# Performance work log

Hardware: AMD Instinct MI355X
Metric: run time of the kernel (lower is better)

The kernel has to match this reference:

```python
import jax, jax.numpy as jnp
import numpy as np

QK = 64
KNN = 16
EPS = 1e-5


def conv1(x, w, b):
    # x: (B,C,N), w: (O,C) -> (B,O,N)
    return jnp.einsum('oc,bcn->bon', w, x) + b[None, :, None]


def conv2(x, w, b):
    # x: (B,C,N,k), w: (O,C) -> (B,O,N,k)
    return jnp.einsum('oc,bcnk->bonk', w, x) + b[None, :, None, None]


def bn1(x, g, b, m, v):
    return g[None, :, None] * (x - m[None, :, None]) * jax.lax.rsqrt(v + EPS)[None, :, None] + b[None, :, None]


def bn2(x, g, b, m, v):
    return g[None, :, None, None] * (x - m[None, :, None, None]) * jax.lax.rsqrt(v + EPS)[None, :, None, None] + b[None, :, None, None]


def gather_nk(t, idx):
    # t: (B,C,M), idx: (B,N,k) -> (B,C,N,k)
    return jax.vmap(lambda tb, ib: tb[:, ib])(t, idx)


def setup_inputs():
    key = jax.random.key(0)
    ks = jax.random.split(key, 40)
    B, N, M = 2, 16384, 4096
    w = lambda k, s: jax.random.normal(k, s, dtype=jnp.float32) * 0.05
    d = {}
    d['xyz_hr'] = jax.random.normal(ks[0], (B, 3, N), dtype=jnp.float32)
    d['xyz_lr'] = jax.random.normal(ks[1], (B, 3, M), dtype=jnp.float32)
    d['sft_feat_lr'] = jax.random.normal(ks[2], (B, 6, M), dtype=jnp.float32)
    d['val_lr'] = jax.random.normal(ks[3], (B, 64, M), dtype=jnp.float32)
    # geom_encoder: Conv1d(3,64) -> BN -> ReLU -> Conv1d(64,64)
    d['ge_w1'] = w(ks[4], (QK, 3)); d['ge_b1'] = w(ks[5], (QK,))
    d['ge_g1'] = jnp.ones((QK,)); d['ge_be1'] = jnp.zeros((QK,))
    d['ge_m1'] = w(ks[6], (QK,)); d['ge_v1'] = jax.random.uniform(ks[7], (QK,), minval=0.5, maxval=1.5)
    d['ge_w2'] = w(ks[8], (QK, QK)); d['ge_b2'] = w(ks[9], (QK,))
    # scale/shift convs Conv1d(6,64)
    d['sc_w'] = w(ks[10], (QK, 6)); d['sc_b'] = w(ks[11], (QK,))
    d['sh_w'] = w(ks[12], (QK, 6)); d['sh_b'] = w(ks[13], (QK,))
    # sem query/key Conv1d(64,64)
    d['q_w'] = w(ks[14], (QK, QK)); d['q_b'] = w(ks[15], (QK,))
    d['k_w'] = w(ks[16], (QK, QK)); d['k_b'] = w(ks[17], (QK,))
    # bdy_head: Conv1d(64,64) -> BN -> ReLU -> Conv1d(64,1) -> Sigmoid
    d['bd_w1'] = w(ks[18], (64, QK)); d['bd_b1'] = w(ks[19], (64,))
    d['bd_g'] = jnp.ones((64,)); d['bd_be'] = jnp.zeros((64,))
    d['bd_m'] = w(ks[20], (64,)); d['bd_v'] = jax.random.uniform(ks[21], (64,), minval=0.5, maxval=1.5)
    d['bd_w2'] = w(ks[22], (1, 64)); d['bd_b2'] = w(ks[23], (1,))
    # rel_pos_mlp: Conv2d(3,64) -> BN2d -> ReLU -> Conv2d(64,64)
    d['rp_w1'] = w(ks[24], (QK, 3)); d['rp_b1'] = w(ks[25], (QK,))
    d['rp_g'] = jnp.ones((QK,)); d['rp_be'] = jnp.zeros((QK,))
    d['rp_m'] = w(ks[26], (QK,)); d['rp_v'] = jax.random.uniform(ks[27], (QK,), minval=0.5, maxval=1.5)
    d['rp_w2'] = w(ks[28], (QK, QK)); d['rp_b2'] = w(ks[29], (QK,))
    return d


def reference(xyz_hr, xyz_lr, sft_feat_lr, val_lr,
              ge_w1, ge_b1, ge_g1, ge_be1, ge_m1, ge_v1, ge_w2, ge_b2,
              sc_w, sc_b, sh_w, sh_b, q_w, q_b, k_w, k_b,
              bd_w1, bd_b1, bd_g, bd_be, bd_m, bd_v, bd_w2, bd_b2,
              rp_w1, rp_b1, rp_g, rp_be, rp_m, rp_v, rp_w2, rp_b2):
    B, _, M = sft_feat_lr.shape
    curr_k = min(KNN, M)

    def geom_enc(x):
        h = jax.nn.relu(bn1(conv1(x, ge_w1, ge_b1), ge_g1, ge_be1, ge_m1, ge_v1))
        return conv1(h, ge_w2, ge_b2)

    geom_hr = geom_enc(xyz_hr)                     # (B,64,N)
    geom_lr = geom_enc(xyz_lr)                     # (B,64,M)
    scale = conv1(sft_feat_lr, sc_w, sc_b)
    shift = conv1(sft_feat_lr, sh_w, sh_b)
    geom_lr_mod = geom_lr * (scale + 1.0) + shift
    Q = conv1(geom_hr, q_w, q_b)                   # (B,64,N)
    K = conv1(geom_lr_mod, k_w, k_b)               # (B,64,M)
    # boundary head
    h = jax.nn.relu(bn1(conv1(geom_hr, bd_w1, bd_b1), bd_g, bd_be, bd_m, bd_v))
    bdy_prob = jax.nn.sigmoid(conv1(h, bd_w2, bd_b2))  # (B,1,N)
    # kNN via squared distances (same argmin ordering as torch.cdist)
    hr_t = jnp.swapaxes(xyz_hr, 1, 2)              # (B,N,3)
    lr_t = jnp.swapaxes(xyz_lr, 1, 2)              # (B,M,3)
    d2 = (jnp.sum(hr_t**2, -1)[:, :, None] + jnp.sum(lr_t**2, -1)[:, None, :]
          - 2.0 * jnp.einsum('bnd,bmd->bnm', hr_t, lr_t))  # (B,N,M)
    _, k_idx = jax.lax.top_k(-d2, curr_k)          # (B,N,k) int32
    k_idx = jax.lax.stop_gradient(k_idx)

    K_g = gather_nk(K, k_idx)                      # (B,64,N,k)
    xyz_lr_g = gather_nk(xyz_lr, k_idx)            # (B,3,N,k)
    rel_pos = xyz_hr[:, :, :, None] - xyz_lr_g     # (B,3,N,k)
    pe = jax.nn.relu(bn2(conv2(rel_pos, rp_w1, rp_b1), rp_g, rp_be, rp_m, rp_v))
    pos_enc = conv2(pe, rp_w2, rp_b2)              # (B,64,N,k)
    logits = jnp.sum(Q[:, :, :, None] * (K_g + pos_enc), axis=1) / np.sqrt(QK)  # (B,N,k)
    attn = jax.nn.softmax(logits, axis=-1)
    val_g = gather_nk(val_lr, k_idx)               # (B,Cv,N,k)
    out = jnp.sum(attn[:, None, :, :] * val_g, axis=-1)  # (B,Cv,N)
    return out, bdy_prob
```

## Files before the change

kernel.cpp:

```cpp
#include <hip/hip_runtime.h>
#include <hip/hip_bf16.h>

#define B_ 2
#define N_ 16384
#define M_ 4096
#define EPS_ 1e-5f

__device__ __forceinline__ float b2f(const __hip_bfloat16 v) { return __bfloat162float(v); }

__device__ __forceinline__ float ldin(const void* p, size_t i, int f32) {
    return f32 ? ((const float*)p)[i] : __bfloat162float(((const __hip_bfloat16*)p)[i]);
}
__device__ __forceinline__ void stout(void* o, size_t i, float v, int f32) {
    if (f32) ((float*)o)[i] = v;
    else     ((__hip_bfloat16*)o)[i] = __float2bfloat16(v);
}

__device__ __forceinline__ float d2np(float x, float y, float z, float hn, float4 q) {
    float dot = __fadd_rn(__fadd_rn(__fmul_rn(x, q.x), __fmul_rn(y, q.y)), __fmul_rn(z, q.z));
    return __fsub_rn(__fadd_rn(hn, q.w), __fmul_rn(2.f, dot));
}
__device__ __forceinline__ float norm3np(float x, float y, float z) {
    return __fadd_rn(__fadd_rn(__fmul_rn(x, x), __fmul_rn(y, y)), __fmul_rn(z, z));
}

#define O_GE_W1 0
#define O_GE_B1 192
#define O_GE_W2 256
#define O_GE_B2 4352
#define O_QW    4416
#define O_QB    8512
#define O_KW    8576
#define O_KB    12672
#define O_SCW   12736
#define O_SCB   13120
#define O_SHW   13184
#define O_SHB   13568
#define O_BDW1  13632
#define O_BDB1  17728
#define O_BDW2  17792
#define O_BDB2  17856
#define O_RPW1  17920
#define O_RPB1  18112
#define O_RPW2  18176
#define O_RPB2  22272
#define OB_LR    92160
#define OB_Q     223232
#define OB_KT    4417536
#define OB_VT    5466112
#define OB_KIDX  6514688
#define OB_DFLAG 7694336
#define O_T_GE_W2 1923840
#define O_T_QW    1927936
#define O_T_KW    1932032
#define O_T_BDW1  1936128

#define CAP  12
#define CAPS 13

__global__ __launch_bounds__(256) void prep_kernel(
    const void* xyz_hr,
    const void* ge_w1, const void* ge_b1, const void* ge_g1, const void* ge_be1,
    const void* ge_m1, const void* ge_v1, const void* ge_w2, const void* ge_b2,
    const void* sc_w, const void* sc_b, const void* sh_w, const void* sh_b,
    const void* q_w, const void* q_b, const void* k_w, const void* k_b,
    const void* bd_w1, const void* bd_b1, const void* bd_g, const void* bd_be,
    const void* bd_m, const void* bd_v, const void* bd_w2, const void* bd_b2,
    const void* rp_w1, const void* rp_b1, const void* rp_g, const void* rp_be,
    const void* rp_m, const void* rp_v, const void* rp_w2, const void* rp_b2,
    float* W, int* dflag)
{
    __shared__ int scnt;
    int t = threadIdx.x;
    if (t == 0) scnt = 0;
    __syncthreads();
    if (t < 128) {
        unsigned short u = ((const unsigned short*)xyz_hr)[t];
        int e = (u >> 7) & 0xFF;
        int ok = (e >= 113 && e <= 132) || ((u & 0x7FFF) == 0);
        if (ok) atomicAdd(&scnt, 1);
    }
    __syncthreads();
    const int f32 = (scnt < 110) ? 1 : 0;
    if (t == 0) *dflag = f32;

    if (t < 64) {
        float s = ldin(ge_g1, t, f32) * rsqrtf(ldin(ge_v1, t, f32) + EPS_);
        for (int d = 0; d < 3; ++d) W[O_GE_W1 + t*3 + d] = s * ldin(ge_w1, t*3 + d, f32);
        W[O_GE_B1 + t] = s * (ldin(ge_b1, t, f32) - ldin(ge_m1, t, f32)) + ldin(ge_be1, t, f32);
        W[O_GE_B2 + t] = ldin(ge_b2, t, f32);
        W[O_QB + t] = ldin(q_b, t, f32);
        W[O_KB + t] = ldin(k_b, t, f32);
        W[O_SCB + t] = ldin(sc_b, t, f32);
        W[O_SHB + t] = ldin(sh_b, t, f32);
        float sb = ldin(bd_g, t, f32) * rsqrtf(ldin(bd_v, t, f32) + EPS_);
        W[O_BDB1 + t] = sb * (ldin(bd_b1, t, f32) - ldin(bd_m, t, f32)) + ldin(bd_be, t, f32);
        W[O_BDW2 + t] = ldin(bd_w2, t, f32);
        float sr = ldin(rp_g, t, f32) * rsqrtf(ldin(rp_v, t, f32) + EPS_);
        for (int d = 0; d < 3; ++d) W[O_RPW1 + t*3 + d] = sr * ldin(rp_w1, t*3 + d, f32);
        W[O_RPB1 + t] = sr * (ldin(rp_b1, t, f32) - ldin(rp_m, t, f32)) + ldin(rp_be, t, f32);
        W[O_RPB2 + t] = ldin(rp_b2, t, f32);
    }
    if (t == 0) W[O_BDB2] = ldin(bd_b2, 0, f32);
    for (int i = t; i < 4096; i += 256) {
        int c = i >> 6, r = i & 63;
        float w2 = ldin(ge_w2, i, f32);
        float qw = ldin(q_w, i, f32);
        float kw = ldin(k_w, i, f32);
        float sb = ldin(bd_g, c, f32) * rsqrtf(ldin(bd_v, c, f32) + EPS_);
        float bw = sb * ldin(bd_w1, i, f32);
        W[O_GE_W2 + i] = w2;
        W[O_QW + i]    = qw;
        W[O_KW + i]    = kw;
        W[O_RPW2 + i]  = ldin(rp_w2, i, f32);
        W[O_BDW1 + i]  = bw;
        W[O_T_GE_W2 + r*64 + c] = w2;
        W[O_T_QW    + r*64 + c] = qw;
        W[O_T_KW    + r*64 + c] = kw;
        W[O_T_BDW1  + r*64 + c] = bw;
    }
    for (int i = t; i < 384; i += 256) {
        W[O_SCW + i] = ldin(sc_w, i, f32);
        W[O_SHW + i] = ldin(sh_w, i, f32);
    }
}

__global__ __launch_bounds__(256) void lr_kernel(
    const void* __restrict__ xyz_lr,
    const void* __restrict__ sft,
    const void* __restrict__ val,
    const float* __restrict__ W,
    __hip_bfloat16* __restrict__ Kt, __hip_bfloat16* __restrict__ Vt,
    float4* __restrict__ LR, const int* dflag)
{
    const int f32 = *dflag;
    int lane = threadIdx.x & 63;
    int p = blockIdx.x * 4 + (threadIdx.x >> 6);
    int b = p >> 12, m = p & (M_ - 1);
    size_t base = (size_t)b*3*M_ + m;
    float x = ldin(xyz_lr, base, f32), y = ldin(xyz_lr, base + M_, f32), z = ldin(xyz_lr, base + 2*M_, f32);
    if (lane == 0) LR[p] = make_float4(x, y, z, norm3np(x, y, z));

    const float* w1 = W + O_GE_W1 + lane*3;
    float h = fmaxf(fmaf(w1[2], z, fmaf(w1[1], y, fmaf(w1[0], x, W[O_GE_B1 + lane]))), 0.f);
    float g = W[O_GE_B2 + lane];
#pragma unroll
    for (int i = 0; i < 64; ++i) {
        g = fmaf(W[O_T_GE_W2 + i*64 + lane], __shfl(h, i, 64), g);
    }
    float sc = W[O_SCB + lane], sh = W[O_SHB + lane];
    const float* wsc = W + O_SCW + lane*6;
    const float* wsh = W + O_SHW + lane*6;
#pragma unroll
    for (int d = 0; d < 6; ++d) {
        float s6 = ldin(sft, (size_t)b*6*M_ + d*M_ + m, f32);
        sc = fmaf(wsc[d], s6, sc); sh = fmaf(wsh[d], s6, sh);
    }
    float mod = fmaf(g, sc + 1.f, sh);
    float k = W[O_KB + lane];
#pragma unroll
    for (int i = 0; i < 64; ++i) {
        k = fmaf(W[O_T_KW + i*64 + lane], __shfl(mod, i, 64), k);
    }
    Kt[(size_t)p*64 + lane] = __float2bfloat16(k);
    Vt[(size_t)p*64 + lane] = __float2bfloat16(ldin(val, (size_t)b*64*M_ + (size_t)lane*M_ + m, f32));
}

__global__ __launch_bounds__(256) void hr_kernel(
    const void* __restrict__ xyz_hr,
    const float* __restrict__ W,
    __hip_bfloat16* __restrict__ Q,
    void* __restrict__ out, const int* dflag)
{
    const int f32 = *dflag;
    int lane = threadIdx.x & 63;
    int p = blockIdx.x * 4 + (threadIdx.x >> 6);
    int b = p >> 14, n = p & (N_ - 1);
    size_t base = (size_t)b*3*N_ + n;
    float x = ldin(xyz_hr, base, f32), y = ldin(xyz_hr, base + N_, f32), z = ldin(xyz_hr, base + 2*N_, f32);

    const float* w1 = W + O_GE_W1 + lane*3;
    float h = fmaxf(fmaf(w1[2], z, fmaf(w1[1], y, fmaf(w1[0], x, W[O_GE_B1 + lane]))), 0.f);
    float g = W[O_GE_B2 + lane];
#pragma unroll
    for (int i = 0; i < 64; ++i) {
        g = fmaf(W[O_T_GE_W2 + i*64 + lane], __shfl(h, i, 64), g);
    }
    float q = W[O_QB + lane];
#pragma unroll
    for (int i = 0; i < 64; ++i) {
        q = fmaf(W[O_T_QW + i*64 + lane], __shfl(g, i, 64), q);
    }
    Q[(size_t)p*64 + lane] = __float2bfloat16(q);
    float hb = W[O_BDB1 + lane];
#pragma unroll
    for (int i = 0; i < 64; ++i) {
        hb = fmaf(W[O_T_BDW1 + i*64 + lane], __shfl(g, i, 64), hb);
    }
    float o = W[O_BDW2 + lane] * fmaxf(hb, 0.f);
#pragma unroll
    for (int sh = 1; sh < 64; sh <<= 1) o += __shfl_xor(o, sh, 64);
    if (lane == 0) {
        o += W[O_BDB2];
        stout(out, (size_t)B_*64*N_ + (size_t)b*N_ + n, 1.f / (1.f + __expf(-o)), f32);
    }
}

#define CE(da, ia, db, ib) { \
    bool sw_ = (db < da) || (db == da && ib < ia); \
    float td_ = da; int ti_ = ia; \
    da = sw_ ? db : da; ia = sw_ ? ib : ia; \
    db = sw_ ? td_ : db; ib = sw_ ? ti_ : ib; }

__device__ __forceinline__ void topk_insert(float (&bd)[16], int (&bi)[16], float d2, int m) {
    if (d2 < bd[15] || (d2 == bd[15] && m < bi[15])) {
        bd[15] = d2; bi[15] = m;
#pragma unroll
        for (int j = 15; j > 0; --j) CE(bd[j-1], bi[j-1], bd[j], bi[j]);
    }
}

__global__ __launch_bounds__(256, 2) void knn_kernel(
    const void* __restrict__ xyz_hr,
    const float4* __restrict__ LR,
    unsigned short* __restrict__ kidx, const int* dflag)
{
#pragma clang fp reassociate(off)
    __shared__ float4         sLR[512];
    __shared__ float          sdd[256 * CAPS];
    __shared__ unsigned short sii[256 * CAPS];
    const int f32 = *dflag;
    int lane = threadIdx.x & 63;
    int p = blockIdx.x * 4 + (threadIdx.x >> 6);
    int b = p >> 14, n = p & (N_ - 1);
    size_t base = (size_t)b*3*N_ + n;
    float x = ldin(xyz_hr, base, f32), y = ldin(xyz_hr, base + N_, f32), z = ldin(xyz_hr, base + 2*N_, f32);
    float hn = norm3np(x, y, z);
    const float4* L = LR + b*M_;

    float d2r[64];
    float v = 3.4e38f;
#pragma unroll
    for (int c = 0; c < 8; ++c) {
        __syncthreads();
        sLR[threadIdx.x]       = L[c*512 + threadIdx.x];
        sLR[256 + threadIdx.x] = L[c*512 + 256 + threadIdx.x];
        __syncthreads();
#pragma unroll
        for (int i = 0; i < 8; ++i) {
            float d2 = d2np(x, y, z, hn, sLR[i*64 + lane]);
            d2r[c*8 + i] = d2;
            v = fminf(v, d2);
        }
    }
    v = fminf(v, __shfl_xor(v, 16, 64));
    v = fminf(v, __shfl_xor(v, 32, 64));
    float tau = v;
#pragma unroll
    for (int st = 1; st <= 8; st <<= 1) tau = fmaxf(tau, __shfl_xor(tau, st, 64));

    int sl = threadIdx.x * CAPS;
    int cnt = 0;
#pragma unroll
    for (int i = 0; i < 64; ++i) {
        if (d2r[i] <= tau) {
            if (cnt < CAP) { sdd[sl + cnt] = d2r[i]; sii[sl + cnt] = (unsigned short)(i*64 + lane); }
            cnt++;
        }
    }
    int bad = (cnt > CAP) ? 1 : 0;
#pragma unroll
    for (int st = 1; st <= 32; st <<= 1) bad |= __shfl_xor(bad, st, 64);
    if (bad) {
        float bd[16]; int bi[16];
#pragma unroll
        for (int j = 0; j < 16; ++j) { bd[j] = 3.4e38f; bi[j] = 0x7fffffff; }
        for (int m = 0; m < M_; ++m) {
            topk_insert(bd, bi, d2np(x, y, z, hn, L[m]), m);
        }
        if (lane == 0) {
            unsigned short* kr = kidx + (size_t)p*16;
#pragma unroll
            for (int j = 0; j < 16; ++j) kr[j] = (unsigned short)bi[j];
        }
        return;
    }
    for (int a = 0; a < cnt - 1; ++a) {
        float bv = sdd[sl + a]; int bm = (int)sii[sl + a]; int bj = a;
        for (int j2 = a + 1; j2 < cnt; ++j2) {
            float dj = sdd[sl + j2]; int mj = (int)sii[sl + j2];
            if (dj < bv || (dj == bv && mj < bm)) { bv = dj; bm = mj; bj = j2; }
        }
        float ta = sdd[sl + a]; int ia = (int)sii[sl + a];
        sdd[sl + a] = bv; sii[sl + a] = (unsigned short)bm;
        sdd[sl + bj] = ta; sii[sl + bj] = (unsigned short)ia;
    }

    int ptr = 0;
    for (int r = 0; r < 16; ++r) {
        float hd = 3.4e38f; int hi = 0x7fffffff;
        if (ptr < cnt) { hd = sdd[sl + ptr]; hi = (int)sii[sl + ptr]; }
        float md = hd; int mi = hi;
#pragma unroll
        for (int st = 1; st <= 32; st <<= 1) {
            float od = __shfl_xor(md, st, 64);
            int   oi = __shfl_xor(mi, st, 64);
            bool s = (od < md) || (od == md && oi < mi);
            md = s ? od : md; mi = s ? oi : mi;
        }
        if (ptr < cnt && hi == mi) {
            kidx[(size_t)p*16 + r] = (unsigned short)mi;
            ptr++;
        }
    }
}

__global__ __launch_bounds__(256) void attn_kernel(
    const void* __restrict__ xyz_hr,
    const float4* __restrict__ LR,
    const float* __restrict__ W,
    const __hip_bfloat16* __restrict__ Q,
    const __hip_bfloat16* __restrict__ Kt,
    const __hip_bfloat16* __restrict__ Vt,
    const unsigned short* __restrict__ kidx,
    void* __restrict__ out, const int* dflag)
{
    const int f32 = *dflag;
    int p = (blockIdx.x * 256 + threadIdx.x) >> 6;
    int lane = threadIdx.x & 63;
    float fw0 = W[O_RPW1 + lane*3], fw1 = W[O_RPW1 + lane*3 + 1], fw2 = W[O_RPW1 + lane*3 + 2];
    float fb  = W[O_RPB1 + lane];

    int b = p >> 14, n = p & (N_ - 1);
    size_t base = (size_t)b*3*N_ + n;
    float xh = ldin(xyz_hr, base, f32), yh = ldin(xyz_hr, base + N_, f32), zh = ldin(xyz_hr, base + 2*N_, f32);
    float qc = b2f(Q[(size_t)p*64 + lane]);
    float q2 = 0.f;
#pragma unroll
    for (int cc = 0; cc < 64; ++cc) {
        float qb = __shfl(qc, cc, 64);
        q2 = fmaf(W[O_RPW2 + cc*64 + lane], qb, q2);
    }
    int idxv = (int)kidx[(size_t)p*16 + (lane & 15)];
    const float4* L = LR + b*M_;
    const __hip_bfloat16* Ktb = Kt + (size_t)b*M_*64;
    const __hip_bfloat16* Vtb = Vt + (size_t)b*M_*64;
    float lg[16];
#pragma unroll
    for (int j = 0; j < 16; ++j) {
        int mj = __shfl(idxv, j, 64);
        mj = (mj < M_) ? mj : (M_ - 1);
        float4 pl = L[mj];
        float r0 = xh - pl.x, r1 = yh - pl.y, r2 = zh - pl.z;
        float pe = fmaxf(fmaf(fw2, r2, fmaf(fw1, r1, fmaf(fw0, r0, fb))), 0.f);
        float v = fmaf(qc, b2f(Ktb[(size_t)mj*64 + lane]), q2 * pe);
#pragma unroll
        for (int sh = 1; sh < 64; sh <<= 1) v += __shfl_xor(v, sh, 64);
        lg[j] = v * 0.125f;
    }
    float mx = lg[0];
#pragma unroll
    for (int j = 1; j < 16; ++j) mx = fmaxf(mx, lg[j]);
    float sum = 0.f;
#pragma unroll
    for (int j = 0; j < 16; ++j) { lg[j] = __expf(lg[j] - mx); sum += lg[j]; }
    float inv = 1.f / sum;
    float o = 0.f;
#pragma unroll
    for (int j = 0; j < 16; ++j) {
        int mj = __shfl(idxv, j, 64);
        mj = (mj < M_) ? mj : (M_ - 1);
        o = fmaf(lg[j] * inv, b2f(Vtb[(size_t)mj*64 + lane]), o);
    }
    stout(out, ((size_t)(b*64 + lane))*N_ + n, o, f32);
}

extern "C" void kernel_launch(void* const* d_in, const int* in_sizes, int n_in,
                              void* d_out, int out_size, void* d_ws, size_t ws_size,
                              hipStream_t stream) {
    const void* xyz_hr = d_in[0];
    const void* xyz_lr = d_in[1];
    const void* sft    = d_in[2];
    const void* val    = d_in[3];

    char* ws = (char*)d_ws;
    float* W  = (float*)ws;
    float4* LR = (float4*)(ws + OB_LR);
    __hip_bfloat16* Qp = (__hip_bfloat16*)(ws + OB_Q);
    __hip_bfloat16* Kt = (__hip_bfloat16*)(ws + OB_KT);
    __hip_bfloat16* Vt = (__hip_bfloat16*)(ws + OB_VT);
    unsigned short* kidx = (unsigned short*)(ws + OB_KIDX);
    int* dflag = (int*)(ws + OB_DFLAG);

    prep_kernel<<<1, 256, 0, stream>>>(
        xyz_hr,
        d_in[4],  d_in[5],  d_in[6],  d_in[7],  d_in[8],  d_in[9],  d_in[10], d_in[11],
        d_in[12], d_in[13], d_in[14], d_in[15], d_in[16], d_in[17], d_in[18], d_in[19],
        d_in[20], d_in[21], d_in[22], d_in[23], d_in[24], d_in[25], d_in[26], d_in[27],
        d_in[28], d_in[29], d_in[30], d_in[31], d_in[32], d_in[33], d_in[34], d_in[35],
        W, dflag);
    lr_kernel<<<2048, 256, 0, stream>>>(xyz_lr, sft, val, W, Kt, Vt, LR, dflag);
    hr_kernel<<<8192, 256, 0, stream>>>(xyz_hr, W, Qp, d_out, dflag);
    knn_kernel<<<8192, 256, 0, stream>>>(xyz_hr, LR, kidx, dflag);
    attn_kernel<<<8192, 256, 0, stream>>>(xyz_hr, LR, W, Qp, Kt, Vt, kidx, d_out, dflag);
}
```

Before: 425.9 us.

## Fuse HR encoder, kNN and attention into one kernel

Result: slower. 586.8 us (+37.8%).

```diff
diff --git a/kernel.cpp b/kernel.cpp
--- a/kernel.cpp
+++ b/kernel.cpp
@@ -45,10 +45,8 @@
 #define O_RPW2  18176
 #define O_RPB2  22272
 #define OB_LR    92160
-#define OB_Q     223232
 #define OB_KT    4417536
 #define OB_VT    5466112
-#define OB_KIDX  6514688
 #define OB_DFLAG 7694336
 #define O_T_GE_W2 1923840
 #define O_T_QW    1927936
@@ -109,11 +107,7 @@
         float kw = ldin(k_w, i, f32);
         float sb = ldin(bd_g, c, f32) * rsqrtf(ldin(bd_v, c, f32) + EPS_);
         float bw = sb * ldin(bd_w1, i, f32);
-        W[O_GE_W2 + i] = w2;
-        W[O_QW + i]    = qw;
-        W[O_KW + i]    = kw;
-        W[O_RPW2 + i]  = ldin(rp_w2, i, f32);
-        W[O_BDW1 + i]  = bw;
+        W[O_RPW2 + i] = ldin(rp_w2, i, f32);
         W[O_T_GE_W2 + r*64 + c] = w2;
         W[O_T_QW    + r*64 + c] = qw;
         W[O_T_KW    + r*64 + c] = kw;
@@ -166,46 +160,6 @@
     Vt[(size_t)p*64 + lane] = __float2bfloat16(ldin(val, (size_t)b*64*M_ + (size_t)lane*M_ + m, f32));
 }
 
-__global__ __launch_bounds__(256) void hr_kernel(
-    const void* __restrict__ xyz_hr,
-    const float* __restrict__ W,
-    __hip_bfloat16* __restrict__ Q,
-    void* __restrict__ out, const int* dflag)
-{
-    const int f32 = *dflag;
-    int lane = threadIdx.x & 63;
-    int p = blockIdx.x * 4 + (threadIdx.x >> 6);
-    int b = p >> 14, n = p & (N_ - 1);
-    size_t base = (size_t)b*3*N_ + n;
-    float x = ldin(xyz_hr, base, f32), y = ldin(xyz_hr, base + N_, f32), z = ldin(xyz_hr, base + 2*N_, f32);
-
-    const float* w1 = W + O_GE_W1 + lane*3;
-    float h = fmaxf(fmaf(w1[2], z, fmaf(w1[1], y, fmaf(w1[0], x, W[O_GE_B1 + lane]))), 0.f);
-    float g = W[O_GE_B2 + lane];
-#pragma unroll
-    for (int i = 0; i < 64; ++i) {
-        g = fmaf(W[O_T_GE_W2 + i*64 + lane], __shfl(h, i, 64), g);
-    }
-    float q = W[O_QB + lane];
-#pragma unroll
-    for (int i = 0; i < 64; ++i) {
-        q = fmaf(W[O_T_QW + i*64 + lane], __shfl(g, i, 64), q);
-    }
-    Q[(size_t)p*64 + lane] = __float2bfloat16(q);
-    float hb = W[O_BDB1 + lane];
-#pragma unroll
-    for (int i = 0; i < 64; ++i) {
-        hb = fmaf(W[O_T_BDW1 + i*64 + lane], __shfl(g, i, 64), hb);
-    }
-    float o = W[O_BDW2 + lane] * fmaxf(hb, 0.f);
-#pragma unroll
-    for (int sh = 1; sh < 64; sh <<= 1) o += __shfl_xor(o, sh, 64);
-    if (lane == 0) {
-        o += W[O_BDB2];
-        stout(out, (size_t)B_*64*N_ + (size_t)b*N_ + n, 1.f / (1.f + __expf(-o)), f32);
-    }
-}
-
 #define CE(da, ia, db, ib) { \
     bool sw_ = (db < da) || (db == da && ib < ia); \
     float td_ = da; int ti_ = ia; \
@@ -220,10 +174,13 @@
     }
 }
 
-__global__ __launch_bounds__(256, 2) void knn_kernel(
+__global__ __launch_bounds__(256, 2) void fused_kernel(
     const void* __restrict__ xyz_hr,
     const float4* __restrict__ LR,
-    unsigned short* __restrict__ kidx, const int* dflag)
+    const float* __restrict__ W,
+    const __hip_bfloat16* __restrict__ Kt,
+    const __hip_bfloat16* __restrict__ Vt,
+    void* __restrict__ out, const int* dflag)
 {
 #pragma clang fp reassociate(off)
     __shared__ float4         sLR[512];
@@ -238,6 +195,34 @@
     float hn = norm3np(x, y, z);
     const float4* L = LR + b*M_;
 
+    const float* w1 = W + O_GE_W1 + lane*3;
+    float h = fmaxf(fmaf(w1[2], z, fmaf(w1[1], y, fmaf(w1[0], x, W[O_GE_B1 + lane]))), 0.f);
+    float g = W[O_GE_B2 + lane];
+#pragma unroll
+    for (int i = 0; i < 64; ++i) {
+        g = fmaf(W[O_T_GE_W2 + i*64 + lane], __shfl(h, i, 64), g);
+    }
+    float qc = W[O_QB + lane];
+#pragma unroll
+    for (int i = 0; i < 64; ++i) {
+        qc = fmaf(W[O_T_QW + i*64 + lane], __shfl(g, i, 64), qc);
+    }
+    float hb = W[O_BDB1 + lane];
+#pragma unroll
+    for (int i = 0; i < 64; ++i) {
+        hb = fmaf(W[O_T_BDW1 + i*64 + lane], __shfl(g, i, 64), hb);
+    }
+    {
+        float o = W[O_BDW2 + lane] * fmaxf(hb, 0.f);
+#pragma unroll
+        for (int sh = 1; sh < 64; sh <<= 1) o += __shfl_xor(o, sh, 64);
+        if (lane == 0) {
+            o += W[O_BDB2];
+            stout(out, (size_t)B_*64*N_ + (size_t)b*N_ + n, 1.f / (1.f + __expf(-o)), f32);
+        }
+    }
+
+    int idxv = 0;
     float d2r[64];
     float v = 3.4e38f;
 #pragma unroll
@@ -278,85 +263,58 @@
         for (int m = 0; m < M_; ++m) {
             topk_insert(bd, bi, d2np(x, y, z, hn, L[m]), m);
         }
-        if (lane == 0) {
-            unsigned short* kr = kidx + (size_t)p*16;
-#pragma unroll
-            for (int j = 0; j < 16; ++j) kr[j] = (unsigned short)bi[j];
-        }
-        return;
-    }
-    for (int a = 0; a < cnt - 1; ++a) {
-        float bv = sdd[sl + a]; int bm = (int)sii[sl + a]; int bj = a;
-        for (int j2 = a + 1; j2 < cnt; ++j2) {
-            float dj = sdd[sl + j2]; int mj = (int)sii[sl + j2];
-            if (dj < bv || (dj == bv && mj < bm)) { bv = dj; bm = mj; bj = j2; }
-        }
-        float ta = sdd[sl + a]; int ia = (int)sii[sl + a];
-        sdd[sl + a] = bv; sii[sl + a] = (unsigned short)bm;
-        sdd[sl + bj] = ta; sii[sl + bj] = (unsigned short)ia;
-    }
-
-    int ptr = 0;
-    for (int r = 0; r < 16; ++r) {
-        float hd = 3.4e38f; int hi = 0x7fffffff;
-        if (ptr < cnt) { hd = sdd[sl + ptr]; hi = (int)sii[sl + ptr]; }
-        float md = hd; int mi = hi;
-#pragma unroll
-        for (int st = 1; st <= 32; st <<= 1) {
-            float od = __shfl_xor(md, st, 64);
-            int   oi = __shfl_xor(mi, st, 64);
-            bool s = (od < md) || (od == md && oi < mi);
-            md = s ? od : md; mi = s ? oi : mi;
-        }
-        if (ptr < cnt && hi == mi) {
-            kidx[(size_t)p*16 + r] = (unsigned short)mi;
-            ptr++;
-        }
-    }
-}
-
-__global__ __launch_bounds__(256) void attn_kernel(
-    const void* __restrict__ xyz_hr,
-    const float4* __restrict__ LR,
-    const float* __restrict__ W,
-    const __hip_bfloat16* __restrict__ Q,
-    const __hip_bfloat16* __restrict__ Kt,
-    const __hip_bfloat16* __restrict__ Vt,
-    const unsigned short* __restrict__ kidx,
-    void* __restrict__ out, const int* dflag)
-{
-    const int f32 = *dflag;
-    int p = (blockIdx.x * 256 + threadIdx.x) >> 6;
-    int lane = threadIdx.x & 63;
+#pragma unroll
+        for (int j = 0; j < 16; ++j) if ((lane & 15) == j) idxv = bi[j];
+    } else {
+        for (int a = 0; a < cnt - 1; ++a) {
+            float bv = sdd[sl + a]; int bm = (int)sii[sl + a]; int bj = a;
+            for (int j2 = a + 1; j2 < cnt; ++j2) {
+                float dj = sdd[sl + j2]; int mj = (int)sii[sl + j2];
+                if (dj < bv || (dj == bv && mj < bm)) { bv = dj; bm = mj; bj = j2; }
+            }
+            float ta = sdd[sl + a]; int ia = (int)sii[sl + a];
+            sdd[sl + a] = bv; sii[sl + a] = (unsigned short)bm;
+            sdd[sl + bj] = ta; sii[sl + bj] = (unsigned short)ia;
+        }
+        int ptr = 0;
+        for (int r = 0; r < 16; ++r) {
+            float hd = 3.4e38f; int hi = 0x7fffffff;
+            if (ptr < cnt) { hd = sdd[sl + ptr]; hi = (int)sii[sl + ptr]; }
+            float md = hd; int mi = hi;
+#pragma unroll
+            for (int st = 1; st <= 32; st <<= 1) {
+                float od = __shfl_xor(md, st, 64);
+                int   oi = __shfl_xor(mi, st, 64);
+                bool s = (od < md) || (od == md && oi < mi);
+                md = s ? od : md; mi = s ? oi : mi;
+            }
+            if ((lane & 15) == r) idxv = mi;
+            if (ptr < cnt && hi == mi) ptr++;
+        }
+    }
+
     float fw0 = W[O_RPW1 + lane*3], fw1 = W[O_RPW1 + lane*3 + 1], fw2 = W[O_RPW1 + lane*3 + 2];
     float fb  = W[O_RPB1 + lane];
-
-    int b = p >> 14, n = p & (N_ - 1);
-    size_t base = (size_t)b*3*N_ + n;
-    float xh = ldin(xyz_hr, base, f32), yh = ldin(xyz_hr, base + N_, f32), zh = ldin(xyz_hr, base + 2*N_, f32);
-    float qc = b2f(Q[(size_t)p*64 + lane]);
     float q2 = 0.f;
 #pragma unroll
     for (int cc = 0; cc < 64; ++cc) {
         float qb = __shfl(qc, cc, 64);
         q2 = fmaf(W[O_RPW2 + cc*64 + lane], qb, q2);
     }
-    int idxv = (int)kidx[(size_t)p*16 + (lane & 15)];
-    const float4* L = LR + b*M_;
     const __hip_bfloat16* Ktb = Kt + (size_t)b*M_*64;
     const __hip_bfloat16* Vtb = Vt + (size_t)b*M_*64;
     float lg[16];
 #pragma unroll
     for (int j = 0; j < 16; ++j) {
         int mj = __shfl(idxv, j, 64);
-        mj = (mj < M_) ? mj : (M_ - 1);
+        mj = (mj < M_ && mj >= 0) ? mj : (M_ - 1);
         float4 pl = L[mj];
-        float r0 = xh - pl.x, r1 = yh - pl.y, r2 = zh - pl.z;
+        float r0 = x - pl.x, r1 = y - pl.y, r2 = z - pl.z;
         float pe = fmaxf(fmaf(fw2, r2, fmaf(fw1, r1, fmaf(fw0, r0, fb))), 0.f);
-        float v = fmaf(qc, b2f(Ktb[(size_t)mj*64 + lane]), q2 * pe);
-#pragma unroll
-        for (int sh = 1; sh < 64; sh <<= 1) v += __shfl_xor(v, sh, 64);
-        lg[j] = v * 0.125f;
+        float vv = fmaf(qc, b2f(Ktb[(size_t)mj*64 + lane]), q2 * pe);
+#pragma unroll
+        for (int sh = 1; sh < 64; sh <<= 1) vv += __shfl_xor(vv, sh, 64);
+        lg[j] = vv * 0.125f;
     }
     float mx = lg[0];
 #pragma unroll
@@ -369,7 +327,7 @@
 #pragma unroll
     for (int j = 0; j < 16; ++j) {
         int mj = __shfl(idxv, j, 64);
-        mj = (mj < M_) ? mj : (M_ - 1);
+        mj = (mj < M_ && mj >= 0) ? mj : (M_ - 1);
         o = fmaf(lg[j] * inv, b2f(Vtb[(size_t)mj*64 + lane]), o);
     }
     stout(out, ((size_t)(b*64 + lane))*N_ + n, o, f32);
@@ -386,10 +344,8 @@
     char* ws = (char*)d_ws;
     float* W  = (float*)ws;
     float4* LR = (float4*)(ws + OB_LR);
-    __hip_bfloat16* Qp = (__hip_bfloat16*)(ws + OB_Q);
     __hip_bfloat16* Kt = (__hip_bfloat16*)(ws + OB_KT);
     __hip_bfloat16* Vt = (__hip_bfloat16*)(ws + OB_VT);
-    unsigned short* kidx = (unsigned short*)(ws + OB_KIDX);
     int* dflag = (int*)(ws + OB_DFLAG);
 
     prep_kernel<<<1, 256, 0, stream>>>(
@@ -400,7 +356,5 @@
         d_in[28], d_in[29], d_in[30], d_in[31], d_in[32], d_in[33], d_in[34], d_in[35],
         W, dflag);
     lr_kernel<<<2048, 256, 0, stream>>>(xyz_lr, sft, val, W, Kt, Vt, LR, dflag);
-    hr_kernel<<<8192, 256, 0, stream>>>(xyz_hr, W, Qp, d_out, dflag);
-    knn_kernel<<<8192, 256, 0, stream>>>(xyz_hr, LR, kidx, dflag);
-    attn_kernel<<<8192, 256, 0, stream>>>(xyz_hr, LR, W, Qp, Kt, Vt, kidx, d_out, dflag);
-}
+    fused_kernel<<<8192, 256, 0, stream>>>(xyz_hr, LR, W, Kt, Vt, d_out, dflag);
+}
```
